# Kernel optimization log

Hardware: AMD Instinct MI355X
Metric: run time of the kernel (lower is better)

## Reference

```python
import jax, jax.numpy as jnp
import numpy as np


def setup_inputs() -> dict:
    key = jax.random.key(0)
    k1, k2, k3 = jax.random.split(key, 3)
    N, C, H, W, O = 4, 256, 64, 64, 256
    x = jax.random.normal(k1, (N, C, H, W), jnp.float32)
    # offset per forward signature: [N, H*W, 2*3*3]
    offset = jax.random.normal(k2, (N, H * W, 18), jnp.float32)
    # DeformConv weight [O, C, 3, 3], normal_init std=0.01, bias=False
    weight = jax.random.normal(k3, (O, C, 3, 3), jnp.float32) * 0.01
    return {"x": x, "offset": offset, "weight": weight}


def _deform_conv3x3(x, offset, weight):
    """Deformable conv v1: 3x3, stride 1, padding 1, dilation 1, no bias.
    x: [N,C,H,W]; offset: [N,HW,18] (permuted to [N,18,H,W] as in the module);
    weight: [O,C,3,3].
    """
    N, C, H, W = x.shape
    O = weight.shape[0]
    # module does offset.permute(0,2,1).reshape(N,-1,H,W) -> [N,18,H,W]
    off = offset.transpose(0, 2, 1).reshape(N, 9, 2, H, W)  # (dy,dx) per kernel pos
    dy, dx = off[:, :, 0], off[:, :, 1]                      # [N,9,H,W]

    # base 3x3 kernel offsets (padding=1 keeps the grid centered)
    ky = jnp.array([-1, -1, -1, 0, 0, 0, 1, 1, 1], x.dtype)
    kx = jnp.array([-1, 0, 1, -1, 0, 1, -1, 0, 1], x.dtype)
    hg = jnp.arange(H, dtype=x.dtype)[:, None]  # [H,1]
    wg = jnp.arange(W, dtype=x.dtype)[None, :]  # [1,W]
    py = hg[None, None] + ky[None, :, None, None] + dy  # [N,9,H,W] sample rows
    px = wg[None, None] + kx[None, :, None, None] + dx  # [N,9,H,W] sample cols

    y0 = jnp.floor(py)
    x0 = jnp.floor(px)
    wy = (py - y0)[:, None]  # [N,1,9,H,W]
    wx = (px - x0)[:, None]

    def gather(iy, ix):
        # zero-padded gather: out[n,c,k,h,w] = x[n,c,iy,ix] (0 if out of bounds)
        valid = (iy >= 0) & (iy < H) & (ix >= 0) & (ix < W)
        iyc = jnp.clip(iy, 0, H - 1).astype(jnp.int32)
        ixc = jnp.clip(ix, 0, W - 1).astype(jnp.int32)
        g = jax.vmap(lambda xn, yn, wn: xn[:, yn, wn])(x, iyc, ixc)  # [N,C,9,H,W]
        return g * valid[:, None].astype(x.dtype)

    v00 = gather(y0, x0)
    v01 = gather(y0, x0 + 1)
    v10 = gather(y0 + 1, x0)
    v11 = gather(y0 + 1, x0 + 1)
    # bilinear blend -> sampled columns [N,C,9,H,W]
    val = (v00 * (1 - wy) * (1 - wx) + v01 * (1 - wy) * wx
           + v10 * wy * (1 - wx) + v11 * wy * wx)
    # conv accumulate over channels and kernel positions
    return jnp.einsum('nckhw,ock->nohw', val, weight.reshape(O, C, 9))


def reference(x, offset, weight):
    return _deform_conv3x3(x, offset, weight)
```

## Files before the change

### kernel.cpp

```cpp
#include <hip/hip_runtime.h>
#include <hip/hip_fp16.h>

#define CC 256
#define OO 256
#define HH 64
#define WW 64
#define HWN 4096
#define MPB 64
#define NPB 128
#define KCH 128
#define VST 264
#define WST 136

typedef _Float16 half8 __attribute__((ext_vector_type(8)));
typedef _Float16 half2v __attribute__((ext_vector_type(2)));
typedef float f32x4 __attribute__((ext_vector_type(4)));

__device__ __forceinline__ half2v u2h(unsigned u) {
  half2v h; __builtin_memcpy(&h, &u, 4); return h;
}
__device__ __forceinline__ unsigned h2u(half2v h) {
  unsigned u; __builtin_memcpy(&u, &h, 4); return u;
}
__device__ __forceinline__ unsigned short f2h(float f) {
  _Float16 h = (_Float16)f;
  unsigned short us; __builtin_memcpy(&us, &h, 2);
  return us;
}
__device__ __forceinline__ unsigned dupu(unsigned short us) {
  return ((unsigned)us << 16) | us;
}
__device__ __forceinline__ unsigned pk2(float a, float b) {
  half2v h = {(_Float16)a, (_Float16)b};
  return h2u(h);
}

__global__ __launch_bounds__(256) void prep_kernel(
    const float* __restrict__ x, const float* __restrict__ w,
    _Float16* __restrict__ xt, _Float16* __restrict__ wt) {
  __shared__ float tile[64][65];
  const int bid = blockIdx.x;
  const int tid = threadIdx.x;
  if (bid < 1024) {
    const int n  = bid >> 8;
    const int c0 = ((bid >> 6) & 3) * 64;
    const int s0 = (bid & 63) * 64;
    {
      int r  = tid >> 2;
      int sc = (tid & 3) * 16;
      const float* xp = x + ((size_t)(n * CC + c0 + r)) * HWN + s0 + sc;
      *(float4*)&tile[r][sc]      = *(const float4*)(xp);
      *(float4*)&tile[r][sc + 4]  = *(const float4*)(xp + 4);
      *(float4*)&tile[r][sc + 8]  = *(const float4*)(xp + 8);
      *(float4*)&tile[r][sc + 12] = *(const float4*)(xp + 12);
    }
    __syncthreads();
    {
      int s  = tid >> 2;
      int cg = (tid & 3) * 16;
      uint4 u0, u1;
      u0.x = pk2(tile[cg + 0][s],  tile[cg + 1][s]);
      u0.y = pk2(tile[cg + 2][s],  tile[cg + 3][s]);
      u0.z = pk2(tile[cg + 4][s],  tile[cg + 5][s]);
      u0.w = pk2(tile[cg + 6][s],  tile[cg + 7][s]);
      u1.x = pk2(tile[cg + 8][s],  tile[cg + 9][s]);
      u1.y = pk2(tile[cg + 10][s], tile[cg + 11][s]);
      u1.z = pk2(tile[cg + 12][s], tile[cg + 13][s]);
      u1.w = pk2(tile[cg + 14][s], tile[cg + 15][s]);
      _Float16* op = xt + ((size_t)(n * HWN + s0 + s)) * CC + c0 + cg;
      *(uint4*)(op)     = u0;
      *(uint4*)(op + 8) = u1;
    }
  } else {
    int e = (bid - 1024) * 256 + tid;
    int k = e >> 16;
    int o = (e >> 8) & 255;
    int c = e & 255;
    wt[e] = (_Float16)w[((size_t)o * CC + c) * 9 + k];
  }
}

__global__ __launch_bounds__(256, 2) void deform_mfma_kernel(
    const _Float16* __restrict__ xt,
    const _Float16* __restrict__ wt,
    const float* __restrict__ off,
    float* __restrict__ out) {
  __shared__ __align__(16) _Float16 val_lds[MPB * VST];
  __shared__ __align__(16) _Float16 w_lds[NPB * WST];
  __shared__ ushort4 s_po[MPB * 9];
  __shared__ ushort4 s_pw[MPB * 9];

  const int tid  = threadIdx.x;
  const int lane = tid & 63;
  const int wv   = tid >> 6;
  const int n15  = lane & 15;
  const int quad = lane >> 4;

  const int bx    = blockIdx.x;
  const int nb    = (bx & 7) >> 1;
  const int hw0   = (bx >> 3) * MPB;
  const int obase = (bx & 1) * NPB;

  for (int e = tid; e < MPB * 9; e += 256) {
    int p = e / 9;
    int k = e - p * 9;
    int hw = hw0 + p;
    int h = hw >> 6, w = hw & 63;
    size_t ob = ((size_t)(nb * HWN + hw)) * 18 + 2 * k;
    float2 d = *(const float2*)(off + ob);
    float py = (float)(h + k / 3 - 1) + d.x;
    float px = (float)(w + k % 3 - 1) + d.y;
    float fy = floorf(py), fx = floorf(px);
    int iy = (int)fy, ix = (int)fx;
    float wy = py - fy, wx = px - fx;
    float my0 = ((unsigned)iy       < (unsigned)HH) ? 1.f : 0.f;
    float my1 = ((unsigned)(iy + 1) < (unsigned)HH) ? 1.f : 0.f;
    float mx0 = ((unsigned)ix       < (unsigned)WW) ? 1.f : 0.f;
    float mx1 = ((unsigned)(ix + 1) < (unsigned)WW) ? 1.f : 0.f;
    int iy0 = min(max(iy, 0), HH - 1), iy1 = min(max(iy + 1, 0), HH - 1);
    int ix0 = min(max(ix, 0), WW - 1), ix1 = min(max(ix + 1, 0), WW - 1);
    s_po[e] = make_ushort4((unsigned short)(iy0 * WW + ix0),
                           (unsigned short)(iy0 * WW + ix1),
                           (unsigned short)(iy1 * WW + ix0),
                           (unsigned short)(iy1 * WW + ix1));
    s_pw[e] = make_ushort4(f2h((1.f - wy) * (1.f - wx) * my0 * mx0),
                           f2h((1.f - wy) * wx         * my0 * mx1),
                           f2h(wy         * (1.f - wx) * my1 * mx0),
                           f2h(wy         * wx         * my1 * mx1));
  }

  f32x4 acc[4][2];
#pragma unroll
  for (int a = 0; a < 4; ++a)
#pragma unroll
    for (int b = 0; b < 2; ++b) acc[a][b] = (f32x4){0.f, 0.f, 0.f, 0.f};

  const _Float16* xb = xt + (size_t)nb * HWN * CC;
  const int j = lane & 31;
  const int ph = lane >> 5;

  for (int k = 0; k < 9; ++k) {
    __syncthreads();

#pragma unroll
    for (int i = 0; i < 8; ++i) {
      int p = i * 8 + wv * 2 + ph;
      int idx = p * 9 + k;
      ushort4 o4 = s_po[idx];
      ushort4 hw4 = s_pw[idx];
      half2v w00 = u2h(dupu(hw4.x)), w01 = u2h(dupu(hw4.y));
      half2v w10 = u2h(dupu(hw4.z)), w11 = u2h(dupu(hw4.w));
      const _Float16* cb = xb + (size_t)j * 8;
      uint4 v00 = *(const uint4*)(cb + (size_t)o4.x * CC);
      uint4 v01 = *(const uint4*)(cb + (size_t)o4.y * CC);
      uint4 v10 = *(const uint4*)(cb + (size_t)o4.z * CC);
      uint4 v11 = *(const uint4*)(cb + (size_t)o4.w * CC);
      uint4 r;
      r.x = h2u(u2h(v00.x) * w00 + u2h(v01.x) * w01 + u2h(v10.x) * w10 + u2h(v11.x) * w11);
      r.y = h2u(u2h(v00.y) * w00 + u2h(v01.y) * w01 + u2h(v10.y) * w10 + u2h(v11.y) * w11);
      r.z = h2u(u2h(v00.z) * w00 + u2h(v01.z) * w01 + u2h(v10.z) * w10 + u2h(v11.z) * w11);
      r.w = h2u(u2h(v00.w) * w00 + u2h(v01.w) * w01 + u2h(v10.w) * w10 + u2h(v11.w) * w11);
      *(uint4*)(val_lds + p * VST + j * 8) = r;
    }

    for (int cc = 0; cc < CC / KCH; ++cc) {
      __syncthreads();
      {
        int q = tid & 3;
        int orow = tid >> 2;
#pragma unroll
        for (int rr = 0; rr < 2; ++rr) {
          int o = rr * 64 + orow;
          const uint4* src = (const uint4*)(wt + ((size_t)(k * OO + obase + o)) * CC + cc * KCH + q * 32);
          uint4* dst = (uint4*)(w_lds + o * WST + q * 32);
          dst[0] = src[0];
          dst[1] = src[1];
          dst[2] = src[2];
          dst[3] = src[3];
        }
      }
      __syncthreads();
#pragma unroll
      for (int ks = 0; ks < 4; ++ks) {
        int cbase = cc * KCH + ks * 32;
        half8 afr[4], bfr[2];
#pragma unroll
        for (int mt = 0; mt < 4; ++mt)
          afr[mt] = *(const half8*)(val_lds + (mt * 16 + n15) * VST + cbase + quad * 8);
#pragma unroll
        for (int nt = 0; nt < 2; ++nt)
          bfr[nt] = *(const half8*)(w_lds + (wv * 32 + nt * 16 + n15) * WST + ks * 32 + quad * 8);
#pragma unroll
        for (int mt = 0; mt < 4; ++mt)
#pragma unroll
          for (int nt = 0; nt < 2; ++nt)
            acc[mt][nt] = __builtin_amdgcn_mfma_f32_16x16x32_f16(
                afr[mt], bfr[nt], acc[mt][nt], 0, 0, 0);
      }
    }
  }

#pragma unroll
  for (int mt = 0; mt < 4; ++mt)
#pragma unroll
    for (int nt = 0; nt < 2; ++nt) {
      int o  = obase + wv * 32 + nt * 16 + n15;
      int px = hw0 + mt * 16 + quad * 4;
      *(f32x4*)(out + ((size_t)nb * OO + o) * HWN + px) = acc[mt][nt];
    }
}

extern "C" void kernel_launch(void* const* d_in, const int* in_sizes, int n_in,
                              void* d_out, int out_size, void* d_ws, size_t ws_size,
                              hipStream_t stream) {
  const float* x   = (const float*)d_in[0];
  const float* off = (const float*)d_in[1];
  const float* w   = (const float*)d_in[2];
  float* out = (float*)d_out;

  _Float16* wt = (_Float16*)d_ws;
  _Float16* xt = wt + 589824;

  prep_kernel<<<1024 + 2304, 256, 0, stream>>>(x, w, xt, wt);
  deform_mfma_kernel<<<(4 * HWN / MPB) * (OO / NPB), 256, 0, stream>>>(xt, wt, off, out);
}
```

Before: 127.5 us.

## Store sampled values and weights in LDS as pre-swizzled MFMA fragments

Reorganizes both LDS buffers into fragment-major layout: each 512-half block holds one 16x32 MFMA operand tile laid out lane-contiguously, so fragment reads become linear 16-byte per-lane loads with no bank conflicts and no padding. The bilinear gather is remapped so each lane handles one pixel and one quad of channels, looping over 8 channel groups, with outputs written directly in fragment order. Weight staging is likewise rewritten to load fragment-shaped rows. The gather now reads 64-byte strided chunks per pixel row instead of fully coalesced 512-byte rows, which may reduce global load efficiency.

```diff
diff --git a/kernel.cpp b/kernel.cpp
--- a/kernel.cpp
+++ b/kernel.cpp
@@ -9,8 +9,6 @@
 #define MPB 64
 #define NPB 128
 #define KCH 128
-#define VST 264
-#define WST 136
 
 typedef _Float16 half8 __attribute__((ext_vector_type(8)));
 typedef _Float16 half2v __attribute__((ext_vector_type(2)));
@@ -85,8 +83,8 @@
     const _Float16* __restrict__ wt,
     const float* __restrict__ off,
     float* __restrict__ out) {
-  __shared__ __align__(16) _Float16 val_lds[MPB * VST];
-  __shared__ __align__(16) _Float16 w_lds[NPB * WST];
+  __shared__ __align__(16) _Float16 val_lds[32 * 512];
+  __shared__ __align__(16) _Float16 w_lds[32 * 512];
   __shared__ ushort4 s_po[MPB * 9];
   __shared__ ushort4 s_pw[MPB * 9];
 
@@ -136,60 +134,57 @@
     for (int b = 0; b < 2; ++b) acc[a][b] = (f32x4){0.f, 0.f, 0.f, 0.f};
 
   const _Float16* xb = xt + (size_t)nb * HWN * CC;
-  const int j = lane & 31;
-  const int ph = lane >> 5;
+  const int p = wv * 16 + n15;
 
   for (int k = 0; k < 9; ++k) {
     __syncthreads();
 
-#pragma unroll
-    for (int i = 0; i < 8; ++i) {
-      int p = i * 8 + wv * 2 + ph;
+    {
       int idx = p * 9 + k;
       ushort4 o4 = s_po[idx];
       ushort4 hw4 = s_pw[idx];
       half2v w00 = u2h(dupu(hw4.x)), w01 = u2h(dupu(hw4.y));
       half2v w10 = u2h(dupu(hw4.z)), w11 = u2h(dupu(hw4.w));
-      const _Float16* cb = xb + (size_t)j * 8;
-      uint4 v00 = *(const uint4*)(cb + (size_t)o4.x * CC);
-      uint4 v01 = *(const uint4*)(cb + (size_t)o4.y * CC);
-      uint4 v10 = *(const uint4*)(cb + (size_t)o4.z * CC);
-      uint4 v11 = *(const uint4*)(cb + (size_t)o4.w * CC);
-      uint4 r;
-      r.x = h2u(u2h(v00.x) * w00 + u2h(v01.x) * w01 + u2h(v10.x) * w10 + u2h(v11.x) * w11);
-      r.y = h2u(u2h(v00.y) * w00 + u2h(v01.y) * w01 + u2h(v10.y) * w10 + u2h(v11.y) * w11);
-      r.z = h2u(u2h(v00.z) * w00 + u2h(v01.z) * w01 + u2h(v10.z) * w10 + u2h(v11.z) * w11);
-      r.w = h2u(u2h(v00.w) * w00 + u2h(v01.w) * w01 + u2h(v10.w) * w10 + u2h(v11.w) * w11);
-      *(uint4*)(val_lds + p * VST + j * 8) = r;
-    }
-
+      const _Float16* p00 = xb + (size_t)o4.x * CC + quad * 8;
+      const _Float16* p01 = xb + (size_t)o4.y * CC + quad * 8;
+      const _Float16* p10 = xb + (size_t)o4.z * CC + quad * 8;
+      const _Float16* p11 = xb + (size_t)o4.w * CC + quad * 8;
+#pragma unroll
+      for (int g = 0; g < 8; ++g) {
+        uint4 v00 = *(const uint4*)(p00 + g * 32);
+        uint4 v01 = *(const uint4*)(p01 + g * 32);
+        uint4 v10 = *(const uint4*)(p10 + g * 32);
+        uint4 v11 = *(const uint4*)(p11 + g * 32);
+        uint4 r;
+        r.x = h2u(u2h(v00.x) * w00 + u2h(v01.x) * w01 + u2h(v10.x) * w10 + u2h(v11.x) * w11);
+        r.y = h2u(u2h(v00.y) * w00 + u2h(v01.y) * w01 + u2h(v10.y) * w10 + u2h(v11.y) * w11);
+        r.z = h2u(u2h(v00.z) * w00 + u2h(v01.z) * w01 + u2h(v10.z) * w10 + u2h(v11.z) * w11);
+        r.w = h2u(u2h(v00.w) * w00 + u2h(v01.w) * w01 + u2h(v10.w) * w10 + u2h(v11.w) * w11);
+        *(uint4*)(val_lds + (g * 4 + wv) * 512 + lane * 8) = r;
+      }
+    }
+
+    const _Float16* wkb = wt + ((size_t)(k * OO + obase)) * CC;
     for (int cc = 0; cc < CC / KCH; ++cc) {
       __syncthreads();
-      {
-        int q = tid & 3;
-        int orow = tid >> 2;
-#pragma unroll
-        for (int rr = 0; rr < 2; ++rr) {
-          int o = rr * 64 + orow;
-          const uint4* src = (const uint4*)(wt + ((size_t)(k * OO + obase + o)) * CC + cc * KCH + q * 32);
-          uint4* dst = (uint4*)(w_lds + o * WST + q * 32);
-          dst[0] = src[0];
-          dst[1] = src[1];
-          dst[2] = src[2];
-          dst[3] = src[3];
-        }
+#pragma unroll
+      for (int fi = 0; fi < 8; ++fi) {
+        int fb = wv * 8 + fi;
+        int ot = fb >> 2, ks = fb & 3;
+        const uint4* src = (const uint4*)(wkb + ((size_t)(ot * 16 + n15)) * CC +
+                                          cc * KCH + ks * 32 + quad * 8);
+        *(uint4*)(w_lds + fb * 512 + lane * 8) = *src;
       }
       __syncthreads();
 #pragma unroll
       for (int ks = 0; ks < 4; ++ks) {
-        int cbase = cc * KCH + ks * 32;
         half8 afr[4], bfr[2];
 #pragma unroll
         for (int mt = 0; mt < 4; ++mt)
-          afr[mt] = *(const half8*)(val_lds + (mt * 16 + n15) * VST + cbase + quad * 8);
+          afr[mt] = *(const half8*)(val_lds + ((cc * 4 + ks) * 4 + mt) * 512 + lane * 8);
 #pragma unroll
         for (int nt = 0; nt < 2; ++nt)
-          bfr[nt] = *(const half8*)(w_lds + (wv * 32 + nt * 16 + n15) * WST + ks * 32 + quad * 8);
+          bfr[nt] = *(const half8*)(w_lds + ((wv * 2 + nt) * 4 + ks) * 512 + lane * 8);
 #pragma unroll
         for (int mt = 0; mt < 4; ++mt)
 #pragma unroll
```

New measurement: 176.5 us. +38.4%, slower.

## Prefetch weight tiles into registers and issue gather loads before barrier

Applied to the files above, without the earlier changes.

Weight tiles for the next (k, cc) step are now loaded into registers ahead of time and written to LDS from those registers, so global load latency overlaps with the MFMA work. The bilinear gather loads for all 8 pixel rows are issued before the barrier and blended afterwards, which overlaps the random gather latency with other waves finishing the previous MFMA phase. The cost is much higher register pressure (32 uint4 gather values plus 8 uint4 weight values held live), which under launch_bounds(256,2) may cause spills or lower occupancy.

```diff
diff --git a/kernel.cpp b/kernel.cpp
--- a/kernel.cpp
+++ b/kernel.cpp
@@ -128,6 +128,7 @@
                            f2h(wy         * (1.f - wx) * my1 * mx0),
                            f2h(wy         * wx         * my1 * mx1));
   }
+  __syncthreads();
 
   f32x4 acc[4][2];
 #pragma unroll
@@ -136,48 +137,65 @@
     for (int b = 0; b < 2; ++b) acc[a][b] = (f32x4){0.f, 0.f, 0.f, 0.f};
 
   const _Float16* xb = xt + (size_t)nb * HWN * CC;
-  const int j = lane & 31;
+  const int j  = lane & 31;
   const int ph = lane >> 5;
+  const int q    = tid & 3;
+  const int orow = tid >> 2;
+
+  uint4 breg[8];
+  auto bld = [&](int kk, int cc) {
+#pragma unroll
+    for (int rr = 0; rr < 2; ++rr) {
+      const uint4* src = (const uint4*)(wt + ((size_t)(kk * OO + obase + rr * 64 + orow)) * CC +
+                                        cc * KCH + q * 32);
+#pragma unroll
+      for (int jj = 0; jj < 4; ++jj) breg[rr * 4 + jj] = src[jj];
+    }
+  };
+
+  bld(0, 0);
 
   for (int k = 0; k < 9; ++k) {
-    __syncthreads();
-
+    uint4 ld[8][4];
 #pragma unroll
     for (int i = 0; i < 8; ++i) {
       int p = i * 8 + wv * 2 + ph;
-      int idx = p * 9 + k;
-      ushort4 o4 = s_po[idx];
-      ushort4 hw4 = s_pw[idx];
+      ushort4 o4 = s_po[p * 9 + k];
+      const _Float16* cb = xb + (size_t)j * 8;
+      ld[i][0] = *(const uint4*)(cb + (size_t)o4.x * CC);
+      ld[i][1] = *(const uint4*)(cb + (size_t)o4.y * CC);
+      ld[i][2] = *(const uint4*)(cb + (size_t)o4.z * CC);
+      ld[i][3] = *(const uint4*)(cb + (size_t)o4.w * CC);
+    }
+
+    __syncthreads();
+
+#pragma unroll
+    for (int i = 0; i < 8; ++i) {
+      int p = i * 8 + wv * 2 + ph;
+      ushort4 hw4 = s_pw[p * 9 + k];
       half2v w00 = u2h(dupu(hw4.x)), w01 = u2h(dupu(hw4.y));
       half2v w10 = u2h(dupu(hw4.z)), w11 = u2h(dupu(hw4.w));
-      const _Float16* cb = xb + (size_t)j * 8;
-      uint4 v00 = *(const uint4*)(cb + (size_t)o4.x * CC);
-      uint4 v01 = *(const uint4*)(cb + (size_t)o4.y * CC);
-      uint4 v10 = *(const uint4*)(cb + (size_t)o4.z * CC);
-      uint4 v11 = *(const uint4*)(cb + (size_t)o4.w * CC);
       uint4 r;
-      r.x = h2u(u2h(v00.x) * w00 + u2h(v01.x) * w01 + u2h(v10.x) * w10 + u2h(v11.x) * w11);
-      r.y = h2u(u2h(v00.y) * w00 + u2h(v01.y) * w01 + u2h(v10.y) * w10 + u2h(v11.y) * w11);
-      r.z = h2u(u2h(v00.z) * w00 + u2h(v01.z) * w01 + u2h(v10.z) * w10 + u2h(v11.z) * w11);
-      r.w = h2u(u2h(v00.w) * w00 + u2h(v01.w) * w01 + u2h(v10.w) * w10 + u2h(v11.w) * w11);
+      r.x = h2u(u2h(ld[i][0].x) * w00 + u2h(ld[i][1].x) * w01 + u2h(ld[i][2].x) * w10 + u2h(ld[i][3].x) * w11);
+      r.y = h2u(u2h(ld[i][0].y) * w00 + u2h(ld[i][1].y) * w01 + u2h(ld[i][2].y) * w10 + u2h(ld[i][3].y) * w11);
+      r.z = h2u(u2h(ld[i][0].z) * w00 + u2h(ld[i][1].z) * w01 + u2h(ld[i][2].z) * w10 + u2h(ld[i][3].z) * w11);
+      r.w = h2u(u2h(ld[i][0].w) * w00 + u2h(ld[i][1].w) * w01 + u2h(ld[i][2].w) * w10 + u2h(ld[i][3].w) * w11);
       *(uint4*)(val_lds + p * VST + j * 8) = r;
     }
 
     for (int cc = 0; cc < CC / KCH; ++cc) {
       __syncthreads();
       {
-        int q = tid & 3;
-        int orow = tid >> 2;
 #pragma unroll
         for (int rr = 0; rr < 2; ++rr) {
-          int o = rr * 64 + orow;
-          const uint4* src = (const uint4*)(wt + ((size_t)(k * OO + obase + o)) * CC + cc * KCH + q * 32);
-          uint4* dst = (uint4*)(w_lds + o * WST + q * 32);
-          dst[0] = src[0];
-          dst[1] = src[1];
-          dst[2] = src[2];
-          dst[3] = src[3];
+          uint4* dst = (uint4*)(w_lds + (rr * 64 + orow) * WST + q * 32);
+#pragma unroll
+          for (int jj = 0; jj < 4; ++jj) dst[jj] = breg[rr * 4 + jj];
         }
+        int nk = (cc == 0) ? k : k + 1;
+        int ncc = cc ^ 1;
+        if (nk < 9) bld(nk, ncc);
       }
       __syncthreads();
 #pragma unroll
```

Measured after the change: 181.4 us. +42.3%, slower.
